# Kernel tuning notes

Hardware: AMD Instinct MI355X
Metric: run time of the kernel (lower is better)

## Reference

```python
import jax, jax.numpy as jnp
import numpy as np

ITEMS_TOTAL = 50000
DIM = 64
BATCH = 16
N_PER_GRAPH = 50


def setup_inputs() -> dict:
    key = jax.random.key(0)
    k1, k2, k3, k4 = jax.random.split(key, 4)
    nodes = jax.random.randint(k1, (BATCH * N_PER_GRAPH,), 0, ITEMS_TOTAL, dtype=jnp.int64)
    nodes_output = jax.random.normal(k2, (BATCH * N_PER_GRAPH, DIM), dtype=jnp.float32)
    emb_table = jax.random.normal(k3, (ITEMS_TOTAL, DIM), dtype=jnp.float32)
    alpha = jax.random.uniform(k4, (ITEMS_TOTAL, 1), dtype=jnp.float32)  # torch.rand init
    return {"nodes": nodes, "nodes_output": nodes_output, "emb_table": emb_table,
            "alpha": alpha, "n_per_graph": N_PER_GRAPH}


def reference(nodes, nodes_output, emb_table, alpha, n_per_graph):
    items_total, dim = emb_table.shape
    n = int(n_per_graph)
    b = nodes.shape[0] // n
    idx_b = nodes.reshape(b, n)            # (B, n) item indices per graph
    feat_b = nodes_output.reshape(b, n, dim)  # (B, n, F)

    def per_graph(idx, feat):
        # beta: 1 for items present in this graph, 0 otherwise
        beta = jnp.zeros((items_total, 1), dtype=emb_table.dtype).at[idx].set(1.0)
        # gate the full table: untouched rows keep emb, touched rows scaled by (1-alpha)
        embed = (1.0 - beta * alpha) * emb_table          # (items_total, F)
        updated = embed[idx] + alpha[idx] * feat          # (n, F)
        return embed.at[idx].set(updated)

    return jax.vmap(per_graph)(idx_b, feat_b)             # (B, items_total, F)
```

## Files before the change

### kernel.cpp

```cpp
#include <hip/hip_runtime.h>


#define DIM 64
#define SEGS (DIM / 4)
#define BLOCK 256
#define KF 5
#define TILE (BLOCK * KF)
#define NROWS (TILE / SEGS)

__global__ __launch_bounds__(BLOCK) void ggu_stream(
    const int* __restrict__ nodes,
    const float4* __restrict__ feat,
    const float4* __restrict__ emb,
    const float* __restrict__ alpha,
    float4* __restrict__ out,
    int items, int n)
{
    const int b = blockIdx.x;
    const size_t rowsF4 = (size_t)items * SEGS;
    const size_t base   = (size_t)blockIdx.y * TILE;
    const int row0      = (int)(base / SEGS);

    __shared__ int lastj[NROWS];
    for (int i = threadIdx.x; i < NROWS; i += BLOCK) lastj[i] = -1;
    __syncthreads();
    for (int j = threadIdx.x; j < n; j += BLOCK) {
        const int local = nodes[b * n + j] - row0;
        if ((unsigned)local < (unsigned)NROWS)
            atomicMax(&lastj[local], j);
    }
    __syncthreads();

    const float4* e = emb + base;
    float4* o = out + (size_t)b * rowsF4 + base;

    #pragma unroll
    for (int k = 0; k < KF; ++k) {
        const int off = k * BLOCK + (int)threadIdx.x;
        if (base + (size_t)off < rowsF4) {
            float4 v = e[off];
            const int jl = lastj[off >> 4];
            if (jl >= 0) {
                const int row = row0 + (off >> 4);
                const float a = alpha[row];
                const float4 f = feat[(size_t)(b * n + jl) * SEGS + (off & (SEGS - 1))];
                const float om = 1.0f - a;
                v.x = om * v.x + a * f.x;
                v.y = om * v.y + a * f.y;
                v.z = om * v.z + a * f.z;
                v.w = om * v.w + a * f.w;
            }
            o[off] = v;
        }
    }
}

extern "C" void kernel_launch(void* const* d_in, const int* in_sizes, int n_in,
                              void* d_out, int out_size, void* d_ws, size_t ws_size,
                              hipStream_t stream) {
    const int*   nodes = (const int*)d_in[0];
    const float* feat  = (const float*)d_in[1];
    const float* emb   = (const float*)d_in[2];
    const float* alpha = (const float*)d_in[3];

    const int items = in_sizes[3];
    const int B     = out_size / (items * DIM);
    const int n     = in_sizes[0] / B;

    const size_t rowsF4 = (size_t)items * SEGS;
    const unsigned gy = (unsigned)((rowsF4 + TILE - 1) / TILE);
    dim3 grid((unsigned)B, gy);

    ggu_stream<<<grid, BLOCK, 0, stream>>>(
        nodes, (const float4*)feat, (const float4*)emb, alpha,
        (float4*)d_out, items, n);
}
```

Before: 239.9 us.

## Split into broadcast-copy kernel plus sparse fixup kernel for touched rows

Replaces the per-batch tiled streaming kernel with two launches. The first reads each embedding row once and writes it to all batch slices, so the table is read once rather than once per batch. The second kernel overwrites only the rows touched in each graph, using a forward scan to apply last-write-wins. This adds a second launch and serialises the tiny fixup behind the bulk write, and the fixup's per-node quadratic duplicate scan runs in only B blocks.

```diff
diff --git a/kernel.cpp b/kernel.cpp
--- a/kernel.cpp
+++ b/kernel.cpp
@@ -4,53 +4,62 @@
 #define DIM 64
 #define SEGS (DIM / 4)
 #define BLOCK 256
-#define KF 5
-#define TILE (BLOCK * KF)
-#define NROWS (TILE / SEGS)
 
-__global__ __launch_bounds__(BLOCK) void ggu_stream(
+typedef float vf4 __attribute__((ext_vector_type(4)));
+
+template <int CB>
+__global__ __launch_bounds__(BLOCK) void ggu_bcast(
+    const vf4* __restrict__ emb,
+    vf4* __restrict__ out,
+    size_t rowsF4, int Brt)
+{
+    const int B = (CB > 0) ? CB : Brt;
+    const size_t g = (size_t)blockIdx.x * BLOCK + threadIdx.x;
+    if (g >= rowsF4) return;
+    const vf4 v = emb[g];
+    vf4* o = out + g;
+    if (CB > 0) {
+        #pragma unroll
+        for (int b = 0; b < CB; ++b) o[(size_t)b * rowsF4] = v;
+    } else {
+        for (int b = 0; b < B; ++b) o[(size_t)b * rowsF4] = v;
+    }
+}
+
+__global__ __launch_bounds__(BLOCK) void ggu_fix(
     const int* __restrict__ nodes,
-    const float4* __restrict__ feat,
-    const float4* __restrict__ emb,
+    const float* __restrict__ feat,
+    const float* __restrict__ emb,
     const float* __restrict__ alpha,
-    float4* __restrict__ out,
+    float* __restrict__ out,
     int items, int n)
 {
-    const int b = blockIdx.x;
-    const size_t rowsF4 = (size_t)items * SEGS;
-    const size_t base   = (size_t)blockIdx.y * TILE;
-    const int row0      = (int)(base / SEGS);
+    const int b  = blockIdx.x;
+    const int jt = threadIdx.x >> 6;
+    const int d  = threadIdx.x & 63;
+    const int NJ = BLOCK / 64;
 
-    __shared__ int lastj[NROWS];
-    for (int i = threadIdx.x; i < NROWS; i += BLOCK) lastj[i] = -1;
-    __syncthreads();
-    for (int j = threadIdx.x; j < n; j += BLOCK) {
-        const int local = nodes[b * n + j] - row0;
-        if ((unsigned)local < (unsigned)NROWS)
-            atomicMax(&lastj[local], j);
-    }
+    __shared__ int ids[256];
+    for (int t = threadIdx.x; t < n && t < 256; t += BLOCK)
+        ids[t] = nodes[b * n + t];
     __syncthreads();
 
-    const float4* e = emb + base;
-    float4* o = out + (size_t)b * rowsF4 + base;
-
-    #pragma unroll
-    for (int k = 0; k < KF; ++k) {
-        const int off = k * BLOCK + (int)threadIdx.x;
-        if (base + (size_t)off < rowsF4) {
-            float4 v = e[off];
-            const int jl = lastj[off >> 4];
-            if (jl >= 0) {
-                const int row = row0 + (off >> 4);
+    for (int j0 = 0; j0 < n; j0 += NJ) {
+        const int j = j0 + jt;
+        if (j < n) {
+            const int row = (n <= 256) ? ids[j] : nodes[b * n + j];
+            bool last = true;
+            for (int j2 = j + 1; j2 < n; ++j2) {
+                const int r2 = (n <= 256) ? ids[j2] : nodes[b * n + j2];
+                last &= (r2 != row);
+            }
+            if (last) {
                 const float a = alpha[row];
-                const float4 f = feat[(size_t)(b * n + jl) * SEGS + (off & (SEGS - 1))];
-                const float om = 1.0f - a;
-                v.x = om * v.x + a * f.x;
-                v.y = om * v.y + a * f.y;
-                v.z = om * v.z + a * f.z;
-                v.w = om * v.w + a * f.w;
+                const float e = emb[(size_t)row * DIM + d];
+                const float f = feat[(size_t)(b * n + j) * DIM + d];
+                out[(size_t)b * items * DIM + (size_t)row * DIM + d] =
+                    (1.0f - a) * e + a * f;
             }
-            o[off] = v;
         }
     }
 }
@@ -68,10 +77,15 @@
     const int n     = in_sizes[0] / B;
 
     const size_t rowsF4 = (size_t)items * SEGS;
-    const unsigned gy = (unsigned)((rowsF4 + TILE - 1) / TILE);
-    dim3 grid((unsigned)B, gy);
+    const unsigned grid1 = (unsigned)((rowsF4 + BLOCK - 1) / BLOCK);
 
-    ggu_stream<<<grid, BLOCK, 0, stream>>>(
-        nodes, (const float4*)feat, (const float4*)emb, alpha,
-        (float4*)d_out, items, n);
+    if (B == 16) {
+        ggu_bcast<16><<<grid1, BLOCK, 0, stream>>>(
+            (const vf4*)emb, (vf4*)d_out, rowsF4, B);
+    } else {
+        ggu_bcast<0><<<grid1, BLOCK, 0, stream>>>(
+            (const vf4*)emb, (vf4*)d_out, rowsF4, B);
+    }
+    ggu_fix<<<B, BLOCK, 0, stream>>>(
+        nodes, feat, emb, alpha, (float*)d_out, items, n);
 }
```

Measured after the change: 247.7 us. 3.2% more time.
